# Kernel optimization log

Hardware: AMD Instinct MI355X
Metric: run time of the kernel (lower is better)

Reference implementation:

```python
import jax, jax.numpy as jnp
import numpy as np

EMBED_SIZE = 1024
HEADS = 16
HEAD_DIM = EMBED_SIZE // HEADS


def setup_inputs() -> dict:
    key = jax.random.key(0)
    ks = jax.random.split(key, 8)
    B, S = 4, 2048
    inp = {
        "values": jax.random.normal(ks[0], (B, S, EMBED_SIZE), dtype=jnp.float32),
        "keys": jax.random.normal(ks[1], (B, S, EMBED_SIZE), dtype=jnp.float32),
        "query": jax.random.normal(ks[2], (B, S, EMBED_SIZE), dtype=jnp.float32),
        "mask": jnp.zeros((B, S), dtype=jnp.int32),  # accepted but unused, as in the original
        # per-head projection weights (nn.Linear(head_dim, head_dim, bias=False)): y = x @ W.T
        "Wv": jax.random.normal(ks[3], (HEAD_DIM, HEAD_DIM), dtype=jnp.float32) / np.sqrt(HEAD_DIM),
        "Wk": jax.random.normal(ks[4], (HEAD_DIM, HEAD_DIM), dtype=jnp.float32) / np.sqrt(HEAD_DIM),
        "Wq": jax.random.normal(ks[5], (HEAD_DIM, HEAD_DIM), dtype=jnp.float32) / np.sqrt(HEAD_DIM),
        # fc_out: nn.Linear(embed_size, embed_size)
        "Wo": jax.random.normal(ks[6], (EMBED_SIZE, EMBED_SIZE), dtype=jnp.float32) / np.sqrt(EMBED_SIZE),
        "bo": jax.random.normal(ks[7], (EMBED_SIZE,), dtype=jnp.float32) * 0.01,
    }
    return inp


def reference(values, keys, query, mask, Wv, Wk, Wq, Wo, bo):
    N, S, _ = query.shape
    # reshape to (N, len, heads, head_dim)
    v = values.reshape(N, S, HEADS, HEAD_DIM)
    k = keys.reshape(N, S, HEADS, HEAD_DIM)
    q = query.reshape(N, S, HEADS, HEAD_DIM)
    # per-head linear projections (shared across heads), y = x @ W.T
    v = jnp.einsum('nlhd,ed->nlhe', v, Wv)
    k = jnp.einsum('nlhd,ed->nlhe', k, Wk)
    q = jnp.einsum('nlhd,ed->nlhe', q, Wq)
    # attention scores: (N, H, Q, K), scaled by sqrt(embed_size) as in the original
    energy = jnp.einsum('nqhd,nkhd->nhqk', q, k)
    attention = jax.nn.softmax(energy / jnp.sqrt(jnp.float32(EMBED_SIZE)), axis=3)
    out = jnp.einsum('nhql,nlhd->nqhd', attention, v).reshape(N, S, EMBED_SIZE)
    out = out @ Wo.T + bo
    return out
```

## Files before the change

kernel.cpp:

```cpp
#include <hip/hip_runtime.h>


typedef __attribute__((ext_vector_type(8))) short short8;
typedef __attribute__((ext_vector_type(4))) float f32x4;
typedef __attribute__((ext_vector_type(16))) float f32x16;
typedef __attribute__((ext_vector_type(4))) unsigned int uint4v;

constexpr int Bn = 4, Sn = 2048, Hn = 16, Dn = 64, En = 1024;
constexpr int HEADELEMS = Bn * Hn * Sn * Dn;

__device__ __forceinline__ unsigned short f2bf(float f) {
  union { float f; unsigned u; } x; x.f = f;
  unsigned u = x.u;
  return (unsigned short)((u + 0x7FFFu + ((u >> 16) & 1u)) >> 16);
}

__device__ __forceinline__ short8 pack8(f32x4 a, f32x4 b) {
  short8 r;
  r[0] = (short)f2bf(a[0]); r[1] = (short)f2bf(a[1]);
  r[2] = (short)f2bf(a[2]); r[3] = (short)f2bf(a[3]);
  r[4] = (short)f2bf(b[0]); r[5] = (short)f2bf(b[1]);
  r[6] = (short)f2bf(b[2]); r[7] = (short)f2bf(b[3]);
  return r;
}

__device__ __forceinline__ float fexp2(float x) {
#if __has_builtin(__builtin_amdgcn_exp2f)
  return __builtin_amdgcn_exp2f(x);
#else
  return exp2f(x);
#endif
}

__device__ __forceinline__ unsigned cvtpk_bf16(float lo, float hi) {
  unsigned r;
  asm("v_cvt_pk_bf16_f32 %0, %1, %2" : "=v"(r) : "v"(lo), "v"(hi));
  return r;
}

__device__ __forceinline__ void gload_lds16(const unsigned short* g, unsigned short* l) {
  __builtin_amdgcn_global_load_lds((const __attribute__((address_space(1))) void*)g,
                                   (__attribute__((address_space(3))) void*)l, 16, 0, 0);
}

__global__ __launch_bounds__(256) void wvo_kernel(
    const float* __restrict__ Wq, const float* __restrict__ Wk,
    const float* __restrict__ Wv, const float* __restrict__ Wo,
    unsigned short* __restrict__ Ut, unsigned short* __restrict__ Mg) {
  __shared__ float lv[4096];
  __shared__ float lwo[4][1024];
  const int bi = blockIdx.x, t = threadIdx.x;
  const int e0 = bi * 4;
  for (int i = t; i < 4096; i += 256) {
    lv[i] = Wv[i];
    lwo[i >> 10][i & 1023] = Wo[e0 * 1024 + i];
  }
  __syncthreads();
  const int lane = t & 63, wid = t >> 6;
#pragma unroll
  for (int e = 0; e < 4; ++e) {
#pragma unroll
    for (int i = 0; i < 4; ++i) {
      const int h = i * 4 + wid, d = lane;
      float acc = 0.f;
      const float* wrow = &lwo[e][h * 64];
#pragma unroll 8
      for (int dp = 0; dp < 64; ++dp) acc += lv[dp * 64 + d] * wrow[dp];
      Ut[(size_t)(e0 + e) * 1024 + h * 64 + d] = f2bf(acc);
    }
  }
  if (bi < 16) {
    const int idx = bi * 256 + t;
    const int d = idx >> 6, c = idx & 63;
    float acc = 0.f;
#pragma unroll 8
    for (int o = 0; o < 64; ++o) acc += Wq[o * 64 + d] * Wk[o * 64 + c];
    Mg[idx] = f2bf(acc * 0.04508422f);
  }
}

__global__ __launch_bounds__(256) void prep_kernel(
    const float* __restrict__ vin, const float* __restrict__ kin,
    const unsigned short* __restrict__ Mg,
    unsigned short* __restrict__ kp, unsigned short* __restrict__ vT) {
  __shared__ alignas(16) unsigned short ldsK[64][72];
  __shared__ alignas(16) unsigned short ldsV[64][72];

  const int blk = blockIdx.x;
  const int st = blk & 31, h = (blk >> 5) & 15, b = blk >> 9;
  const int s0 = st * 64;
  const int t = threadIdx.x;
  const int wid = t >> 6, lane = t & 63, lg = lane >> 4, li = lane & 15;
  const int row = t >> 2, seg = t & 3;
  const int srcoff = (b * Sn + s0 + row) * En + h * 64 + seg * 16;

  {
    const f32x4* ks = reinterpret_cast<const f32x4*>(kin + srcoff);
    *reinterpret_cast<short8*>(&ldsK[row][seg * 16]) = pack8(ks[0], ks[1]);
    *reinterpret_cast<short8*>(&ldsK[row][seg * 16 + 8]) = pack8(ks[2], ks[3]);
    const f32x4* vs = reinterpret_cast<const f32x4*>(vin + srcoff);
    *reinterpret_cast<short8*>(&ldsV[row][seg * 16]) = pack8(vs[0], vs[1]);
    *reinterpret_cast<short8*>(&ldsV[row][seg * 16 + 8]) = pack8(vs[2], vs[3]);
  }
  __syncthreads();

  {
    const int d = lane, sq = wid;
    unsigned short col[16];
#pragma unroll
    for (int jj = 0; jj < 16; ++jj) col[jj] = ldsV[sq * 16 + jj][d];
    short8 o0, o1;
#pragma unroll
    for (int jj = 0; jj < 8; ++jj) { o0[jj] = (short)col[jj]; o1[jj] = (short)col[8 + jj]; }
    unsigned short* dst = vT + ((size_t)((b * Hn + h) * Dn + d)) * Sn + s0 + sq * 16;
    *reinterpret_cast<short8*>(dst) = o0;
    *reinterpret_cast<short8*>(dst + 8) = o1;
  }

  {
    short8 ka0 = *reinterpret_cast<const short8*>(&ldsK[wid * 16 + li][lg * 8]);
    short8 ka1 = *reinterpret_cast<const short8*>(&ldsK[wid * 16 + li][32 + lg * 8]);
    f32x4 acc[4] = {{0,0,0,0},{0,0,0,0},{0,0,0,0},{0,0,0,0}};
#pragma unroll
    for (int cb = 0; cb < 4; ++cb) {
      short8 b0 = *reinterpret_cast<const short8*>(Mg + (cb * 16 + li) * 64 + lg * 8);
      short8 b1 = *reinterpret_cast<const short8*>(Mg + (cb * 16 + li) * 64 + 32 + lg * 8);
      acc[cb] = __builtin_amdgcn_mfma_f32_16x16x32_bf16(ka0, b0, acc[cb], 0, 0, 0);
      acc[cb] = __builtin_amdgcn_mfma_f32_16x16x32_bf16(ka1, b1, acc[cb], 0, 0, 0);
    }
#pragma unroll
    for (int cb = 0; cb < 4; ++cb)
#pragma unroll
      for (int r = 0; r < 4; ++r)
        ldsK[wid * 16 + lg * 4 + r][cb * 16 + li] = f2bf(acc[cb][r]);
  }
  __syncthreads();

  {
    unsigned short* dst = kp + ((size_t)((b * Hn + h) * Sn + s0 + row)) * Dn + seg * 16;
    *reinterpret_cast<short8*>(dst) = *reinterpret_cast<const short8*>(&ldsK[row][seg * 16]);
    *reinterpret_cast<short8*>(dst + 8) = *reinterpret_cast<const short8*>(&ldsK[row][seg * 16 + 8]);
  }
}

__global__ __launch_bounds__(512, 4) void attn_kernel(
    const float* __restrict__ qin, const unsigned short* __restrict__ kp,
    const unsigned short* __restrict__ vT, unsigned short* __restrict__ pv) {
  __shared__ alignas(16) unsigned short ldsK[2][4096];
  __shared__ alignas(16) unsigned short ldsV[2][4096];
  __shared__ float ldsL[8][32];

  const int bid = blockIdx.x;
  const int xcd = bid & 7, j = bid >> 3;
  const int bh = ((j & 7) << 3) + xcd;
  const int qt = j >> 3;
  const int b = bh >> 4, h = bh & 15;

  const int t = threadIdx.x;
  const int wid = t >> 6, lane = t & 63;
  const int c32 = lane & 31, hi = lane >> 5, rx = c32 & 7;
  const int bhS = bh * Sn;
  const int q0 = qt * 256 + wid * 32;

  const int sr = t >> 3, sg = t & 7;
  const unsigned short* ksrc = kp + (size_t)(bhS + sr) * Dn + ((sg ^ (sr & 7)) << 3);
  const unsigned short* vsrc = vT + ((size_t)bh * Dn + sr) * Sn + ((sg ^ (sr & 7)) << 3);

  short8 qb[4];
#pragma unroll
  for (int ks = 0; ks < 4; ++ks) {
    const float* qrow = qin + (size_t)(b * Sn + q0 + c32) * En + h * 64 + ks * 16 + hi * 8;
    f32x4 a = *reinterpret_cast<const f32x4*>(qrow);
    f32x4 c = *reinterpret_cast<const f32x4*>(qrow + 4);
    qb[ks] = pack8(a, c);
  }

  f32x16 o0, o1;
#pragma unroll
  for (int r = 0; r < 16; ++r) { o0[r] = 0.f; o1[r] = 0.f; }
  float l = 0.f;

  auto stage = [&](int buf, int kt) {
    gload_lds16(ksrc + (size_t)kt * 4096, &ldsK[buf][t * 8]);
    gload_lds16(vsrc + kt * 64, &ldsV[buf][t * 8]);
  };

  stage(0, 0);
  __syncthreads();
  int cur = 0;

  for (int kt = 0; kt < 32; ++kt) {
    if (kt < 31) stage(cur ^ 1, kt + 1);

    const unsigned short* Kb = ldsK[cur];
    f32x16 s0, s1;
#pragma unroll
    for (int r = 0; r < 16; ++r) { s0[r] = 0.f; s1[r] = 0.f; }
    __builtin_amdgcn_s_setprio(1);
#pragma unroll
    for (int ks = 0; ks < 4; ++ks) {
      const int ch = (((2 * ks + hi) ^ rx) << 3);
      short8 ka0 = *reinterpret_cast<const short8*>(&Kb[c32 * 64 + ch]);
      short8 ka1 = *reinterpret_cast<const short8*>(&Kb[(32 + c32) * 64 + ch]);
      s0 = __builtin_amdgcn_mfma_f32_32x32x16_bf16(ka0, qb[ks], s0, 0, 0, 0);
      s1 = __builtin_amdgcn_mfma_f32_32x32x16_bf16(ka1, qb[ks], s1, 0, 0, 0);
    }
    __builtin_amdgcn_s_setprio(0);

#pragma unroll
    for (int r = 0; r < 16; ++r) { s0[r] = fexp2(s0[r]); l += s0[r]; }
#pragma unroll
    for (int r = 0; r < 16; ++r) { s1[r] = fexp2(s1[r]); l += s1[r]; }

    short8 pa[4];
#pragma unroll
    for (int s2 = 0; s2 < 2; ++s2) {
      {
        unsigned k0 = cvtpk_bf16(s0[8 * s2 + 0], s0[8 * s2 + 1]);
        unsigned k1 = cvtpk_bf16(s0[8 * s2 + 2], s0[8 * s2 + 3]);
        unsigned k2 = cvtpk_bf16(s0[8 * s2 + 4], s0[8 * s2 + 5]);
        unsigned k3 = cvtpk_bf16(s0[8 * s2 + 6], s0[8 * s2 + 7]);
        asm("v_permlane32_swap_b32 %0, %1" : "+v"(k0), "+v"(k2));
        asm("v_permlane32_swap_b32 %0, %1" : "+v"(k1), "+v"(k3));
        uint4v u; u[0] = k0; u[1] = k1; u[2] = k2; u[3] = k3;
        pa[s2] = __builtin_bit_cast(short8, u);
      }
      {
        unsigned k0 = cvtpk_bf16(s1[8 * s2 + 0], s1[8 * s2 + 1]);
        unsigned k1 = cvtpk_bf16(s1[8 * s2 + 2], s1[8 * s2 + 3]);
        unsigned k2 = cvtpk_bf16(s1[8 * s2 + 4], s1[8 * s2 + 5]);
        unsigned k3 = cvtpk_bf16(s1[8 * s2 + 6], s1[8 * s2 + 7]);
        asm("v_permlane32_swap_b32 %0, %1" : "+v"(k0), "+v"(k2));
        asm("v_permlane32_swap_b32 %0, %1" : "+v"(k1), "+v"(k3));
        uint4v u; u[0] = k0; u[1] = k1; u[2] = k2; u[3] = k3;
        pa[2 + s2] = __builtin_bit_cast(short8, u);
      }
    }

    const unsigned short* Vb = ldsV[cur];
    __builtin_amdgcn_s_setprio(1);
#pragma unroll
    for (int ks2 = 0; ks2 < 4; ++ks2) {
      const int ch = (((2 * ks2 + hi) ^ rx) << 3);
      short8 vb0 = *reinterpret_cast<const short8*>(&Vb[c32 * 64 + ch]);
      short8 vb1 = *reinterpret_cast<const short8*>(&Vb[(32 + c32) * 64 + ch]);
      o0 = __builtin_amdgcn_mfma_f32_32x32x16_bf16(pa[ks2], vb0, o0, 0, 0, 0);
      o1 = __builtin_amdgcn_mfma_f32_32x32x16_bf16(pa[ks2], vb1, o1, 0, 0, 0);
    }
    __builtin_amdgcn_s_setprio(0);

    __syncthreads();
    cur ^= 1;
  }

  l += __shfl_xor(l, 32, 64);
  ldsL[wid][c32] = 1.f / l;
#pragma unroll
  for (int r = 0; r < 16; ++r) {
    const int ql = (r & 3) + 8 * (r >> 2) + 4 * hi;
    const float inv = ldsL[wid][ql];
    unsigned short* dst = pv + ((size_t)(b * Sn + q0 + ql) * Hn + h) * Dn + c32;
    dst[0]  = f2bf(o0[r] * inv);
    dst[32] = f2bf(o1[r] * inv);
  }
}

__global__ __launch_bounds__(256) void ogemm_kernel(
    const unsigned short* __restrict__ pvm, const unsigned short* __restrict__ Ut,
    const float* __restrict__ bo, float* __restrict__ out) {
  __shared__ alignas(16) unsigned short ldsA[2][8192];
  __shared__ alignas(16) unsigned short ldsB[2][8192];

  const int bid = blockIdx.x;
  const int wg = (bid & 7) * 64 + (bid >> 3);
  const int en = wg & 7, mt = wg >> 3;
  const int t = threadIdx.x;
  const int wid = t >> 6, lane = t & 63, lg = lane >> 4, li = lane & 15;
  const int wr = wid >> 1, wc = wid & 1;
  const int m0 = mt * 128, e0 = en * 128;

  f32x4 acc[4][4];
#pragma unroll
  for (int i = 0; i < 4; ++i)
#pragma unroll
    for (int jj = 0; jj < 4; ++jj) acc[i][jj] = f32x4{0, 0, 0, 0};

  const int r0 = t >> 3, G = t & 7;

  auto stage = [&](int buf, int k0) {
#pragma unroll
    for (int rd = 0; rd < 4; ++rd) {
      const int r = r0 + rd * 32;
      const int so = ((G ^ (r & 7)) << 3);
      gload_lds16(pvm + (size_t)(m0 + r) * 1024 + k0 + so, &ldsA[buf][rd * 2048 + t * 8]);
      gload_lds16(Ut + (size_t)(e0 + r) * 1024 + k0 + so, &ldsB[buf][rd * 2048 + t * 8]);
    }
  };

  stage(0, 0);
  __syncthreads();
  int cur = 0;

  for (int kt = 0; kt < 16; ++kt) {
    if (kt < 15) stage(cur ^ 1, (kt + 1) * 64);
#pragma unroll
    for (int kc = 0; kc < 2; ++kc) {
      short8 af[4], bfr[4];
#pragma unroll
      for (int mr = 0; mr < 4; ++mr) {
        const int row = wr * 64 + mr * 16 + li;
        af[mr] = *reinterpret_cast<const short8*>(
            &ldsA[cur][row * 64 + (((kc * 4 + lg) ^ (li & 7)) << 3)]);
      }
#pragma unroll
      for (int nr = 0; nr < 4; ++nr) {
        const int row = wc * 64 + nr * 16 + li;
        bfr[nr] = *reinterpret_cast<const short8*>(
            &ldsB[cur][row * 64 + (((kc * 4 + lg) ^ (li & 7)) << 3)]);
      }
#pragma unroll
      for (int mr = 0; mr < 4; ++mr)
#pragma unroll
        for (int nr = 0; nr < 4; ++nr)
          acc[mr][nr] = __builtin_amdgcn_mfma_f32_16x16x32_bf16(af[mr], bfr[nr], acc[mr][nr], 0, 0, 0);
    }
    __syncthreads();
    cur ^= 1;
  }

#pragma unroll
  for (int nr = 0; nr < 4; ++nr) {
    const int col = e0 + wc * 64 + nr * 16 + li;
    const float bias = bo[col];
#pragma unroll
    for (int mr = 0; mr < 4; ++mr)
#pragma unroll
      for (int r = 0; r < 4; ++r)
        out[(size_t)(m0 + wr * 64 + mr * 16 + lg * 4 + r) * 1024 + col] = acc[mr][nr][r] + bias;
  }
}

extern "C" void kernel_launch(void* const* d_in, const int* in_sizes, int n_in,
                              void* d_out, int out_size, void* d_ws, size_t ws_size,
                              hipStream_t stream) {
  const float* vin = (const float*)d_in[0];
  const float* kin = (const float*)d_in[1];
  const float* qin = (const float*)d_in[2];
  const float* Wv = (const float*)d_in[4];
  const float* Wk = (const float*)d_in[5];
  const float* Wq = (const float*)d_in[6];
  const float* Wo = (const float*)d_in[7];
  const float* bo = (const float*)d_in[8];
  float* out = (float*)d_out;

  unsigned short* kp = (unsigned short*)d_ws;
  unsigned short* vT = kp + HEADELEMS;
  unsigned short* pv = vT + HEADELEMS;
  unsigned short* Ut = pv + HEADELEMS;
  unsigned short* Mg = Ut + En * En;

  wvo_kernel<<<256, 256, 0, stream>>>(Wq, Wk, Wv, Wo, Ut, Mg);
  prep_kernel<<<2048, 256, 0, stream>>>(vin, kin, Mg, kp, vT);
  attn_kernel<<<512, 512, 0, stream>>>(qin, kp, vT, pv);
  ogemm_kernel<<<512, 256, 0, stream>>>(pv, Ut, bo, out);
}
```

Measured before the change: 268.9 us.

## Give each attention wave two 32-row query tiles to reuse K/V fragments

Halves the attention block to 256 threads (4 waves), with each wave handling 64 query rows as two 32-row tiles that share each K and V fragment loaded from LDS. Each thread now issues two global-to-LDS loads each for K and V per stage, and the row-sum and output store handle both tiles. This halves LDS fragment reads per unit of MFMA work, at the cost of roughly doubled accumulator register pressure and fewer waves per block for hiding latency.

```diff
diff --git a/kernel.cpp b/kernel.cpp
--- a/kernel.cpp
+++ b/kernel.cpp
@@ -143,12 +143,12 @@
   }
 }
 
-__global__ __launch_bounds__(512, 4) void attn_kernel(
+__global__ __launch_bounds__(256, 2) void attn_kernel(
     const float* __restrict__ qin, const unsigned short* __restrict__ kp,
     const unsigned short* __restrict__ vT, unsigned short* __restrict__ pv) {
   __shared__ alignas(16) unsigned short ldsK[2][4096];
   __shared__ alignas(16) unsigned short ldsV[2][4096];
-  __shared__ float ldsL[8][32];
+  __shared__ float ldsL[4][64];
 
   const int bid = blockIdx.x;
   const int xcd = bid & 7, j = bid >> 3;
@@ -160,29 +160,36 @@
   const int wid = t >> 6, lane = t & 63;
   const int c32 = lane & 31, hi = lane >> 5, rx = c32 & 7;
   const int bhS = bh * Sn;
-  const int q0 = qt * 256 + wid * 32;
+  const int q0 = qt * 256 + wid * 64;
 
   const int sr = t >> 3, sg = t & 7;
-  const unsigned short* ksrc = kp + (size_t)(bhS + sr) * Dn + ((sg ^ (sr & 7)) << 3);
-  const unsigned short* vsrc = vT + ((size_t)bh * Dn + sr) * Sn + ((sg ^ (sr & 7)) << 3);
-
-  short8 qb[4];
+  const int sgo = ((sg ^ (sr & 7)) << 3);
+  const unsigned short* ksrcA = kp + (size_t)(bhS + sr) * Dn + sgo;
+  const unsigned short* ksrcB = kp + (size_t)(bhS + 32 + sr) * Dn + sgo;
+  const unsigned short* vsrcA = vT + ((size_t)bh * Dn + sr) * Sn + sgo;
+  const unsigned short* vsrcB = vT + ((size_t)bh * Dn + 32 + sr) * Sn + sgo;
+
+  short8 qbA[4], qbB[4];
 #pragma unroll
   for (int ks = 0; ks < 4; ++ks) {
-    const float* qrow = qin + (size_t)(b * Sn + q0 + c32) * En + h * 64 + ks * 16 + hi * 8;
-    f32x4 a = *reinterpret_cast<const f32x4*>(qrow);
-    f32x4 c = *reinterpret_cast<const f32x4*>(qrow + 4);
-    qb[ks] = pack8(a, c);
-  }
-
-  f32x16 o0, o1;
-#pragma unroll
-  for (int r = 0; r < 16; ++r) { o0[r] = 0.f; o1[r] = 0.f; }
-  float l = 0.f;
+    const float* qrA = qin + (size_t)(b * Sn + q0 + c32) * En + h * 64 + ks * 16 + hi * 8;
+    qbA[ks] = pack8(*reinterpret_cast<const f32x4*>(qrA),
+                    *reinterpret_cast<const f32x4*>(qrA + 4));
+    const float* qrB = qrA + (size_t)32 * En;
+    qbB[ks] = pack8(*reinterpret_cast<const f32x4*>(qrB),
+                    *reinterpret_cast<const f32x4*>(qrB + 4));
+  }
+
+  f32x16 oA0, oA1, oB0, oB1;
+#pragma unroll
+  for (int r = 0; r < 16; ++r) { oA0[r] = 0.f; oA1[r] = 0.f; oB0[r] = 0.f; oB1[r] = 0.f; }
+  float lA = 0.f, lB = 0.f;
 
   auto stage = [&](int buf, int kt) {
-    gload_lds16(ksrc + (size_t)kt * 4096, &ldsK[buf][t * 8]);
-    gload_lds16(vsrc + kt * 64, &ldsV[buf][t * 8]);
+    gload_lds16(ksrcA + (size_t)kt * 4096, &ldsK[buf][t * 8]);
+    gload_lds16(ksrcB + (size_t)kt * 4096, &ldsK[buf][2048 + t * 8]);
+    gload_lds16(vsrcA + kt * 64, &ldsV[buf][t * 8]);
+    gload_lds16(vsrcB + kt * 64, &ldsV[buf][2048 + t * 8]);
   };
 
   stage(0, 0);
@@ -193,48 +200,68 @@
     if (kt < 31) stage(cur ^ 1, kt + 1);
 
     const unsigned short* Kb = ldsK[cur];
-    f32x16 s0, s1;
-#pragma unroll
-    for (int r = 0; r < 16; ++r) { s0[r] = 0.f; s1[r] = 0.f; }
+    f32x16 sA0, sA1, sB0, sB1;
+#pragma unroll
+    for (int r = 0; r < 16; ++r) { sA0[r] = 0.f; sA1[r] = 0.f; sB0[r] = 0.f; sB1[r] = 0.f; }
     __builtin_amdgcn_s_setprio(1);
 #pragma unroll
     for (int ks = 0; ks < 4; ++ks) {
       const int ch = (((2 * ks + hi) ^ rx) << 3);
       short8 ka0 = *reinterpret_cast<const short8*>(&Kb[c32 * 64 + ch]);
       short8 ka1 = *reinterpret_cast<const short8*>(&Kb[(32 + c32) * 64 + ch]);
-      s0 = __builtin_amdgcn_mfma_f32_32x32x16_bf16(ka0, qb[ks], s0, 0, 0, 0);
-      s1 = __builtin_amdgcn_mfma_f32_32x32x16_bf16(ka1, qb[ks], s1, 0, 0, 0);
+      sA0 = __builtin_amdgcn_mfma_f32_32x32x16_bf16(ka0, qbA[ks], sA0, 0, 0, 0);
+      sA1 = __builtin_amdgcn_mfma_f32_32x32x16_bf16(ka1, qbA[ks], sA1, 0, 0, 0);
+      sB0 = __builtin_amdgcn_mfma_f32_32x32x16_bf16(ka0, qbB[ks], sB0, 0, 0, 0);
+      sB1 = __builtin_amdgcn_mfma_f32_32x32x16_bf16(ka1, qbB[ks], sB1, 0, 0, 0);
     }
     __builtin_amdgcn_s_setprio(0);
 
-#pragma unroll
-    for (int r = 0; r < 16; ++r) { s0[r] = fexp2(s0[r]); l += s0[r]; }
-#pragma unroll
-    for (int r = 0; r < 16; ++r) { s1[r] = fexp2(s1[r]); l += s1[r]; }
-
-    short8 pa[4];
+    short8 paA[4], paB[4];
+#pragma unroll
+    for (int r = 0; r < 16; ++r) { sA0[r] = fexp2(sA0[r]); lA += sA0[r]; }
+#pragma unroll
+    for (int r = 0; r < 16; ++r) { sA1[r] = fexp2(sA1[r]); lA += sA1[r]; }
 #pragma unroll
     for (int s2 = 0; s2 < 2; ++s2) {
-      {
-        unsigned k0 = cvtpk_bf16(s0[8 * s2 + 0], s0[8 * s2 + 1]);
-        unsigned k1 = cvtpk_bf16(s0[8 * s2 + 2], s0[8 * s2 + 3]);
-        unsigned k2 = cvtpk_bf16(s0[8 * s2 + 4], s0[8 * s2 + 5]);
-        unsigned k3 = cvtpk_bf16(s0[8 * s2 + 6], s0[8 * s2 + 7]);
-        asm("v_permlane32_swap_b32 %0, %1" : "+v"(k0), "+v"(k2));
-        asm("v_permlane32_swap_b32 %0, %1" : "+v"(k1), "+v"(k3));
-        uint4v u; u[0] = k0; u[1] = k1; u[2] = k2; u[3] = k3;
-        pa[s2] = __builtin_bit_cast(short8, u);
-      }
-      {
-        unsigned k0 = cvtpk_bf16(s1[8 * s2 + 0], s1[8 * s2 + 1]);
-        unsigned k1 = cvtpk_bf16(s1[8 * s2 + 2], s1[8 * s2 + 3]);
-        unsigned k2 = cvtpk_bf16(s1[8 * s2 + 4], s1[8 * s2 + 5]);
-        unsigned k3 = cvtpk_bf16(s1[8 * s2 + 6], s1[8 * s2 + 7]);
-        asm("v_permlane32_swap_b32 %0, %1" : "+v"(k0), "+v"(k2));
-        asm("v_permlane32_swap_b32 %0, %1" : "+v"(k1), "+v"(k3));
-        uint4v u; u[0] = k0; u[1] = k1; u[2] = k2; u[3] = k3;
-        pa[2 + s2] = __builtin_bit_cast(short8, u);
-      }
+      unsigned k0 = cvtpk_bf16(sA0[8 * s2 + 0], sA0[8 * s2 + 1]);
+      unsigned k1 = cvtpk_bf16(sA0[8 * s2 + 2], sA0[8 * s2 + 3]);
+      unsigned k2 = cvtpk_bf16(sA0[8 * s2 + 4], sA0[8 * s2 + 5]);
+      unsigned k3 = cvtpk_bf16(sA0[8 * s2 + 6], sA0[8 * s2 + 7]);
+      asm("v_permlane32_swap_b32 %0, %1" : "+v"(k0), "+v"(k2));
+      asm("v_permlane32_swap_b32 %0, %1" : "+v"(k1), "+v"(k3));
+      uint4v u; u[0] = k0; u[1] = k1; u[2] = k2; u[3] = k3;
+      paA[s2] = __builtin_bit_cast(short8, u);
+      unsigned m0 = cvtpk_bf16(sA1[8 * s2 + 0], sA1[8 * s2 + 1]);
+      unsigned m1 = cvtpk_bf16(sA1[8 * s2 + 2], sA1[8 * s2 + 3]);
+      unsigned m2 = cvtpk_bf16(sA1[8 * s2 + 4], sA1[8 * s2 + 5]);
+      unsigned m3 = cvtpk_bf16(sA1[8 * s2 + 6], sA1[8 * s2 + 7]);
+      asm("v_permlane32_swap_b32 %0, %1" : "+v"(m0), "+v"(m2));
+      asm("v_permlane32_swap_b32 %0, %1" : "+v"(m1), "+v"(m3));
+      uint4v w; w[0] = m0; w[1] = m1; w[2] = m2; w[3] = m3;
+      paA[2 + s2] = __builtin_bit_cast(short8, w);
+    }
+#pragma unroll
+    for (int r = 0; r < 16; ++r) { sB0[r] = fexp2(sB0[r]); lB += sB0[r]; }
+#pragma unroll
+    for (int r = 0; r < 16; ++r) { sB1[r] = fexp2(sB1[r]); lB += sB1[r]; }
+#pragma unroll
+    for (int s2 = 0; s2 < 2; ++s2) {
+      unsigned k0 = cvtpk_bf16(sB0[8 * s2 + 0], sB0[8 * s2 + 1]);
+      unsigned k1 = cvtpk_bf16(sB0[8 * s2 + 2], sB0[8 * s2 + 3]);
+      unsigned k2 = cvtpk_bf16(sB0[8 * s2 + 4], sB0[8 * s2 + 5]);
+      unsigned k3 = cvtpk_bf16(sB0[8 * s2 + 6], sB0[8 * s2 + 7]);
+      asm("v_permlane32_swap_b32 %0, %1" : "+v"(k0), "+v"(k2));
+      asm("v_permlane32_swap_b32 %0, %1" : "+v"(k1), "+v"(k3));
+      uint4v u; u[0] = k0; u[1] = k1; u[2] = k2; u[3] = k3;
+      paB[s2] = __builtin_bit_cast(short8, u);
+      unsigned m0 = cvtpk_bf16(sB1[8 * s2 + 0], sB1[8 * s2 + 1]);
+      unsigned m1 = cvtpk_bf16(sB1[8 * s2 + 2], sB1[8 * s2 + 3]);
+      unsigned m2 = cvtpk_bf16(sB1[8 * s2 + 4], sB1[8 * s2 + 5]);
+      unsigned m3 = cvtpk_bf16(sB1[8 * s2 + 6], sB1[8 * s2 + 7]);
+      asm("v_permlane32_swap_b32 %0, %1" : "+v"(m0), "+v"(m2));
+      asm("v_permlane32_swap_b32 %0, %1" : "+v"(m1), "+v"(m3));
+      uint4v w; w[0] = m0; w[1] = m1; w[2] = m2; w[3] = m3;
+      paB[2 + s2] = __builtin_bit_cast(short8, w);
     }
 
     const unsigned short* Vb = ldsV[cur];
@@ -244,8 +271,10 @@
       const int ch = (((2 * ks2 + hi) ^ rx) << 3);
       short8 vb0 = *reinterpret_cast<const short8*>(&Vb[c32 * 64 + ch]);
       short8 vb1 = *reinterpret_cast<const short8*>(&Vb[(32 + c32) * 64 + ch]);
-      o0 = __builtin_amdgcn_mfma_f32_32x32x16_bf16(pa[ks2], vb0, o0, 0, 0, 0);
-      o1 = __builtin_amdgcn_mfma_f32_32x32x16_bf16(pa[ks2], vb1, o1, 0, 0, 0);
+      oA0 = __builtin_amdgcn_mfma_f32_32x32x16_bf16(paA[ks2], vb0, oA0, 0, 0, 0);
+      oA1 = __builtin_amdgcn_mfma_f32_32x32x16_bf16(paA[ks2], vb1, oA1, 0, 0, 0);
+      oB0 = __builtin_amdgcn_mfma_f32_32x32x16_bf16(paB[ks2], vb0, oB0, 0, 0, 0);
+      oB1 = __builtin_amdgcn_mfma_f32_32x32x16_bf16(paB[ks2], vb1, oB1, 0, 0, 0);
     }
     __builtin_amdgcn_s_setprio(0);
 
@@ -253,15 +282,21 @@
     cur ^= 1;
   }
 
-  l += __shfl_xor(l, 32, 64);
-  ldsL[wid][c32] = 1.f / l;
+  lA += __shfl_xor(lA, 32, 64);
+  lB += __shfl_xor(lB, 32, 64);
+  ldsL[wid][c32] = 1.f / lA;
+  ldsL[wid][32 + c32] = 1.f / lB;
 #pragma unroll
   for (int r = 0; r < 16; ++r) {
     const int ql = (r & 3) + 8 * (r >> 2) + 4 * hi;
-    const float inv = ldsL[wid][ql];
-    unsigned short* dst = pv + ((size_t)(b * Sn + q0 + ql) * Hn + h) * Dn + c32;
-    dst[0]  = f2bf(o0[r] * inv);
-    dst[32] = f2bf(o1[r] * inv);
+    const float invA = ldsL[wid][ql];
+    const float invB = ldsL[wid][32 + ql];
+    unsigned short* dA = pv + ((size_t)(b * Sn + q0 + ql) * Hn + h) * Dn + c32;
+    dA[0]  = f2bf(oA0[r] * invA);
+    dA[32] = f2bf(oA1[r] * invA);
+    unsigned short* dB = pv + ((size_t)(b * Sn + q0 + 32 + ql) * Hn + h) * Dn + c32;
+    dB[0]  = f2bf(oB0[r] * invB);
+    dB[32] = f2bf(oB1[r] * invB);
   }
 }
 
@@ -361,6 +396,6 @@
 
   wvo_kernel<<<256, 256, 0, stream>>>(Wq, Wk, Wv, Wo, Ut, Mg);
   prep_kernel<<<2048, 256, 0, stream>>>(vin, kin, Mg, kp, vT);
-  attn_kernel<<<512, 512, 0, stream>>>(qin, kp, vT, pv);
+  attn_kernel<<<512, 256, 0, stream>>>(qin, kp, vT, pv);
   ogemm_kernel<<<512, 256, 0, stream>>>(pv, Ut, bo, out);
 }
```

Result: no change. 265.5 us (-1.3%).
